# Optimization experiments

Hardware: AMD Instinct MI355X
Metric: run time of the kernel (lower is better)

Reference implementation:

```python
import jax, jax.numpy as jnp
import numpy as np

B, S, H, E, V = 128, 400, 256, 128, 50000
PAD = 250  # extended-vocab padding hard-coded in the torch module


def setup_inputs() -> dict:
    key = jax.random.key(0)
    ks = jax.random.split(key, 20)
    return {
        "input_token": jax.random.randint(ks[0], (B, 1), 0, V),
        "last_decoder_hidden": jax.random.normal(ks[1], (B, H), jnp.float32),
        "encoder_states": jax.random.normal(ks[2], (B, S, H), jnp.float32),
        "full_input_var": jax.random.randint(ks[3], (B, S), 0, V + PAD),
        "emb_table": jax.random.normal(ks[4], (V, E), jnp.float32) * 0.02,
        "gru_w_ih": jax.random.normal(ks[5], (3 * H, E), jnp.float32) * 0.05,
        "gru_w_hh": jax.random.normal(ks[6], (3 * H, H), jnp.float32) * 0.05,
        "gru_b_ih": jax.random.normal(ks[7], (3 * H,), jnp.float32) * 0.05,
        "gru_b_hh": jax.random.normal(ks[8], (3 * H,), jnp.float32) * 0.05,
        "w_h": jax.random.normal(ks[9], (H,), jnp.float32),
        "w_s": jax.random.normal(ks[10], (H,), jnp.float32),
        "att_bias": jax.random.normal(ks[11], (1,), jnp.float32),
        "attn_v": jax.random.normal(ks[12], (H,), jnp.float32),
        "gen_w": jax.random.normal(ks[13], (1, 2 * H + E), jnp.float32) * 0.05,
        "gen_b": jax.random.normal(ks[14], (1,), jnp.float32) * 0.05,
        "outh_w": jax.random.normal(ks[15], (E, 2 * H), jnp.float32) * 0.05,
        "outh_b": jax.random.normal(ks[16], (E,), jnp.float32) * 0.05,
        "outv_w": jax.random.normal(ks[17], (V, E), jnp.float32) * 0.05,
        "outv_b": jax.random.normal(ks[18], (V,), jnp.float32) * 0.05,
    }


def reference(input_token, last_decoder_hidden, encoder_states, full_input_var,
              emb_table, gru_w_ih, gru_w_hh, gru_b_ih, gru_b_hh,
              w_h, w_s, att_bias, attn_v, gen_w, gen_b,
              outh_w, outh_b, outv_w, outv_b):
    b, s, h = encoder_states.shape
    v = outv_w.shape[0]
    # Embedding lookup (dropout is identity in eval mode): [B, E]
    x = emb_table[input_token[:, 0]]
    # Single-step GRU cell (PyTorch gate order: r, z, n)
    gi = x @ gru_w_ih.T + gru_b_ih
    gh = last_decoder_hidden @ gru_w_hh.T + gru_b_hh
    i_r, i_z, i_n = jnp.split(gi, 3, axis=-1)
    h_r, h_z, h_n = jnp.split(gh, 3, axis=-1)
    r = jax.nn.sigmoid(i_r + h_r)
    z = jax.nn.sigmoid(i_z + h_z)
    n = jnp.tanh(i_n + r * h_n)
    h_new = (1.0 - z) * n + z * last_decoder_hidden  # [B, H]
    # Bahdanau-style elementwise attention
    att = jnp.tanh(w_h * encoder_states + w_s * h_new[:, None, :] + att_bias)  # [B,S,H]
    scores = jnp.einsum('bsh,h->bs', att, attn_v)
    att_dist = jax.nn.softmax(scores, axis=-1)  # [B, S]
    context = jnp.einsum('bs,bsh->bh', att_dist, encoder_states)  # [B, H]
    dec_ctx = jnp.concatenate([h_new, context], axis=-1)  # [B, 2H]
    p_vocab = jax.nn.softmax((dec_ctx @ outh_w.T + outh_b) @ outv_w.T + outv_b, axis=-1)  # [B, V]
    p_gen = jax.nn.sigmoid(jnp.concatenate([dec_ctx, x], axis=1) @ gen_w.T + gen_b)  # [B, 1]
    # Pointer scatter-add into extended vocab [B, V+PAD]
    rows = jnp.arange(b)[:, None]
    token_input_dist = jnp.zeros((b, v + PAD), p_vocab.dtype).at[rows, full_input_var].add(att_dist)
    p_final = jnp.concatenate([p_vocab * p_gen, jnp.zeros((b, PAD), p_vocab.dtype)], axis=1) \
              + (1.0 - p_gen) * token_input_dist
    return (h_new, p_final, p_gen, p_vocab, att_dist)
```

## Files before the change

### kernel.cpp

```cpp
#include <hip/hip_runtime.h>
#include <hip/hip_bf16.h>


#define B_ 128
#define S_ 400
#define H_ 256
#define E_ 128
#define V_ 50000
#define PAD_ 250
#define VP_ (V_ + PAD_)
#define NC_ 8
#define CS_ (S_ / NC_)
#define NSUM_ 16

typedef unsigned short ushort_t;
typedef __attribute__((ext_vector_type(8))) short bf16x8;
typedef __attribute__((ext_vector_type(4))) float f32x4;

__device__ __forceinline__ unsigned short f2bfu(float f) {
    __hip_bfloat16 h = __float2bfloat16(f);
    union { __hip_bfloat16 h; unsigned short u; } c;
    c.h = h;
    return c.u;
}

__device__ __forceinline__ float sigmoid_fast(float x) {
    return 1.0f / (1.0f + __expf(-x));
}

__device__ __forceinline__ float tanh_fast(float x) {
    return 1.0f - 2.0f / (__expf(2.0f * x) + 1.0f);
}

__device__ __forceinline__ float waveReduceSumAll(float v) {
#pragma unroll
    for (int off = 1; off < 64; off <<= 1) v += __shfl_xor(v, off, 64);
    return v;
}

__global__ __launch_bounds__(256) void k_gates(
    const int* __restrict__ token, const float* __restrict__ emb,
    const float* __restrict__ hprev,
    const float* __restrict__ w_ih, const float* __restrict__ w_hh,
    float* __restrict__ gi_ws, float* __restrict__ gh_ws,
    float* __restrict__ row_sum16) {
    __shared__ ushort_t xh[B_ * 264];
    __shared__ int toks[B_];
    int t = threadIdx.x;
    bool isIH = blockIdx.x < 12;
    if (blockIdx.x == 0) {
        for (int i = t; i < NSUM_ * B_; i += 256) row_sum16[i] = 0.0f;
    }
    if (isIH) {
        if (t < B_) toks[t] = token[t];
        __syncthreads();
#pragma unroll
        for (int i = 0; i < 16; i++) {
            int fidx = i * 256 + t;
            int b = fidx >> 5, k4 = fidx & 31;
            float4 q = *(const float4*)(emb + (size_t)toks[b] * E_ + k4 * 4);
            ushort4 u;
            u.x = f2bfu(q.x); u.y = f2bfu(q.y); u.z = f2bfu(q.z); u.w = f2bfu(q.w);
            *(ushort4*)&xh[b * 136 + k4 * 4] = u;
        }
    } else {
#pragma unroll
        for (int i = 0; i < 32; i++) {
            int fidx = i * 256 + t;
            int b = fidx >> 6, k4 = fidx & 63;
            float4 q = *(const float4*)(hprev + (size_t)b * H_ + k4 * 4);
            ushort4 u;
            u.x = f2bfu(q.x); u.y = f2bfu(q.y); u.z = f2bfu(q.z); u.w = f2bfu(q.w);
            *(ushort4*)&xh[b * 264 + k4 * 4] = u;
        }
    }
    __syncthreads();

    int wave = t >> 6, lane = t & 63, lm = lane & 15, quad = lane >> 4;
    int tile = (isIH ? blockIdx.x : blockIdx.x - 12) * 4 + wave;
    int v = tile * 16 + lm;
    int K = isIH ? E_ : H_;
    int pitch = isIH ? 136 : 264;
    const float* wrow = (isIH ? w_ih : w_hh) + (size_t)v * K;
    float* gout = isIH ? gi_ws : gh_ws;

    f32x4 acc[8];
#pragma unroll
    for (int bt = 0; bt < 8; bt++) acc[bt] = (f32x4){0.f, 0.f, 0.f, 0.f};

    for (int kc = 0; kc < (K >> 5); kc++) {
        int k0 = kc * 32 + quad * 8;
        float4 w0 = *(const float4*)(wrow + k0);
        float4 w1 = *(const float4*)(wrow + k0 + 4);
        bf16x8 bf;
        bf[0] = (short)f2bfu(w0.x); bf[1] = (short)f2bfu(w0.y);
        bf[2] = (short)f2bfu(w0.z); bf[3] = (short)f2bfu(w0.w);
        bf[4] = (short)f2bfu(w1.x); bf[5] = (short)f2bfu(w1.y);
        bf[6] = (short)f2bfu(w1.z); bf[7] = (short)f2bfu(w1.w);
#pragma unroll
        for (int bt = 0; bt < 8; bt++) {
            bf16x8 af = *(const bf16x8*)&xh[(bt * 16 + lm) * pitch + k0];
            acc[bt] = __builtin_amdgcn_mfma_f32_16x16x32_bf16(af, bf, acc[bt], 0, 0, 0);
        }
    }
#pragma unroll
    for (int bt = 0; bt < 8; bt++)
#pragma unroll
        for (int r = 0; r < 4; r++) {
            int b = bt * 16 + quad * 4 + r;
            gout[(size_t)b * 768 + v] = acc[bt][r];
        }
}

__global__ __launch_bounds__(256) void k_attn(
    const float* __restrict__ gi_ws, const float* __restrict__ gh_ws,
    const float* __restrict__ b_ih, const float* __restrict__ b_hh,
    const float* __restrict__ hprev,
    const float* __restrict__ enc,
    const float* __restrict__ w_h, const float* __restrict__ w_s,
    const float* __restrict__ att_bias, const float* __restrict__ attn_v,
    float* __restrict__ out_hnew,
    float* __restrict__ sc_ws, float* __restrict__ ml_ws, float* __restrict__ ctxp_ws) {
    int c = blockIdx.x, b = blockIdx.y;
    int t = threadIdx.x;
    int wave = t >> 6, lane = t & 63;
    __shared__ float whs[H_], vs[H_], cs[H_], cmerge[H_];
    __shared__ float mred[4], lred[4];

    {
        float ir = gi_ws[(size_t)b * 768 + t] + b_ih[t];
        float iz = gi_ws[(size_t)b * 768 + 256 + t] + b_ih[256 + t];
        float in_ = gi_ws[(size_t)b * 768 + 512 + t] + b_ih[512 + t];
        float hr = gh_ws[(size_t)b * 768 + t] + b_hh[t];
        float hz = gh_ws[(size_t)b * 768 + 256 + t] + b_hh[256 + t];
        float hn = gh_ws[(size_t)b * 768 + 512 + t] + b_hh[512 + t];
        float hp = hprev[(size_t)b * H_ + t];
        float r = sigmoid_fast(ir + hr);
        float z = sigmoid_fast(iz + hz);
        float n = tanh_fast(in_ + r * hn);
        float h = (1.0f - z) * n + z * hp;
        if (c == 0) out_hnew[(size_t)b * H_ + t] = h;
        whs[t] = w_h[t];
        vs[t] = attn_v[t];
        cs[t] = w_s[t] * h + att_bias[0];
        cmerge[t] = 0.0f;
    }
    __syncthreads();

    int h0 = lane * 4;
    float wh0 = whs[h0], wh1 = whs[h0 + 1], wh2 = whs[h0 + 2], wh3 = whs[h0 + 3];
    float vv0 = vs[h0], vv1 = vs[h0 + 1], vv2 = vs[h0 + 2], vv3 = vs[h0 + 3];
    float cc0 = cs[h0], cc1 = cs[h0 + 1], cc2 = cs[h0 + 2], cc3 = cs[h0 + 3];

    float m_w = -1e30f, l_w = 0.0f;
    float cx0 = 0.f, cx1 = 0.f, cx2 = 0.f, cx3 = 0.f;
    for (int si = wave; si < CS_; si += 4) {
        int s = c * CS_ + si;
        float4 u = *(const float4*)(enc + ((size_t)(b * S_ + s)) * H_ + h0);
        float p = vv0 * tanh_fast(wh0 * u.x + cc0)
                + vv1 * tanh_fast(wh1 * u.y + cc1)
                + vv2 * tanh_fast(wh2 * u.z + cc2)
                + vv3 * tanh_fast(wh3 * u.w + cc3);
        p = waveReduceSumAll(p);
        if (lane == 0) sc_ws[b * S_ + s] = p;
        float mn = fmaxf(m_w, p);
        float scale = __expf(m_w - mn);
        float w = __expf(p - mn);
        cx0 = cx0 * scale + w * u.x;
        cx1 = cx1 * scale + w * u.y;
        cx2 = cx2 * scale + w * u.z;
        cx3 = cx3 * scale + w * u.w;
        l_w = l_w * scale + w;
        m_w = mn;
    }
    if (lane == 0) mred[wave] = m_w;
    __syncthreads();
    float m_c = fmaxf(fmaxf(mred[0], mred[1]), fmaxf(mred[2], mred[3]));
    float wf = __expf(m_w - m_c);
    if (lane == 0) lred[wave] = l_w * wf;
    atomicAdd(&cmerge[h0 + 0], cx0 * wf);
    atomicAdd(&cmerge[h0 + 1], cx1 * wf);
    atomicAdd(&cmerge[h0 + 2], cx2 * wf);
    atomicAdd(&cmerge[h0 + 3], cx3 * wf);
    __syncthreads();
    if (t == 0) {
        ml_ws[(b * NC_ + c) * 2 + 0] = m_c;
        ml_ws[(b * NC_ + c) * 2 + 1] = lred[0] + lred[1] + lred[2] + lred[3];
    }
    ctxp_ws[(size_t)(b * NC_ + c) * H_ + t] = cmerge[t];
}

__global__ __launch_bounds__(1024) void k_combine(
    const float* __restrict__ sc_ws, const float* __restrict__ ml_ws,
    const float* __restrict__ ctxp_ws,
    const float* __restrict__ out_hnew,
    const int* __restrict__ token, const float* __restrict__ emb,
    const float* __restrict__ outh_w, const float* __restrict__ outh_b,
    const float* __restrict__ gen_w, const float* __restrict__ gen_b,
    float* __restrict__ out_attd, float* __restrict__ out_pgen,
    ushort_t* __restrict__ hidbf_ws) {
    int b = blockIdx.x;
    int t = threadIdx.x;
    int wave = t >> 6, lane = t & 63;
    __shared__ float ml[NC_ * 2];
    __shared__ float dc[2 * H_ + E_];
    __shared__ float r2[16];

    if (t < NC_ * 2) ml[t] = ml_ws[b * NC_ * 2 + t];
    __syncthreads();
    float M = -1e30f;
#pragma unroll
    for (int c = 0; c < NC_; c++) M = fmaxf(M, ml[2 * c]);
    float L = 0.0f;
#pragma unroll
    for (int c = 0; c < NC_; c++) L += ml[2 * c + 1] * __expf(ml[2 * c] - M);
    float invL = 1.0f / L;

    if (t < S_) {
        out_attd[(size_t)b * S_ + t] = __expf(sc_ws[b * S_ + t] - M) * invL;
    }
    if (t < H_) {
        float acc = 0.0f;
#pragma unroll
        for (int c = 0; c < NC_; c++)
            acc += __expf(ml[2 * c] - M) * ctxp_ws[(size_t)(b * NC_ + c) * H_ + t];
        dc[t] = out_hnew[(size_t)b * H_ + t];
        dc[H_ + t] = acc * invL;
    }
    if (t < E_) dc[2 * H_ + t] = emb[(size_t)token[b] * E_ + t];
    __syncthreads();

    {
        int r = t >> 3, sub = t & 7;
        const float* wrow = outh_w + (size_t)r * (2 * H_);
        float acc = 0.0f;
#pragma unroll
        for (int i = 0; i < 16; i++) {
            int k = i * 32 + sub * 4;
            float4 q = *(const float4*)(wrow + k);
            acc += dc[k] * q.x + dc[k + 1] * q.y + dc[k + 2] * q.z + dc[k + 3] * q.w;
        }
        acc += __shfl_down(acc, 4, 64);
        acc += __shfl_down(acc, 2, 64);
        acc += __shfl_down(acc, 1, 64);
        if (sub == 0) hidbf_ws[(size_t)b * E_ + r] = f2bfu(acc + outh_b[r]);
    }
    float pp = (t < 2 * H_ + E_) ? dc[t] * gen_w[t] : 0.0f;
    pp = waveReduceSumAll(pp);
    if (lane == 0) r2[wave] = pp;
    __syncthreads();
    if (t == 0) {
        float g = 0.0f;
#pragma unroll
        for (int wv = 0; wv < 16; wv++) g += r2[wv];
        out_pgen[b] = sigmoid_fast(g + gen_b[0]);
    }
}

#define VT_TOTAL (V_ / 16)
#define HID_PITCH 136

__device__ __forceinline__ void stage_hid(const ushort_t* __restrict__ hidbf_ws,
                                          ushort_t* __restrict__ hid, int t) {
    const uint4* src = (const uint4*)hidbf_ws;
#pragma unroll
    for (int i = 0; i < 16; i++) {
        int i4 = i * 256 + t;
        uint4 q = src[i4];
        int row = i4 >> 4;
        int col4 = (i4 & 15) * 4;
        *(uint4*)&hid[row * HID_PITCH + col4 * 2] = q;
    }
}

__device__ __forceinline__ void vocab_gemm(const ushort_t* __restrict__ hid,
                                           const float* __restrict__ wrow,
                                           int lm, int quad, f32x4 acc[8]) {
#pragma unroll
    for (int kc = 0; kc < 4; kc++) {
        int k0 = kc * 32 + quad * 8;
        float4 w0 = *(const float4*)(wrow + k0);
        float4 w1 = *(const float4*)(wrow + k0 + 4);
        bf16x8 bf;
        bf[0] = (short)f2bfu(w0.x); bf[1] = (short)f2bfu(w0.y);
        bf[2] = (short)f2bfu(w0.z); bf[3] = (short)f2bfu(w0.w);
        bf[4] = (short)f2bfu(w1.x); bf[5] = (short)f2bfu(w1.y);
        bf[6] = (short)f2bfu(w1.z); bf[7] = (short)f2bfu(w1.w);
#pragma unroll
        for (int bt = 0; bt < 8; bt++) {
            bf16x8 af = *(const bf16x8*)&hid[(bt * 16 + lm) * HID_PITCH + k0];
            acc[bt] = __builtin_amdgcn_mfma_f32_16x16x32_bf16(af, bf, acc[bt], 0, 0, 0);
        }
    }
}

__global__ __launch_bounds__(256) void k_vocab_sum(
    const float* __restrict__ outv_w, const float* __restrict__ outv_b,
    const ushort_t* __restrict__ hidbf_ws,
    float* __restrict__ row_sum16) {
    __shared__ ushort_t hid[B_ * HID_PITCH];
    __shared__ float rsum[B_];
    int t = threadIdx.x;
    stage_hid(hidbf_ws, hid, t);
    if (t < B_) rsum[t] = 0.0f;
    __syncthreads();

    int wave = t >> 6, lane = t & 63, lm = lane & 15, quad = lane >> 4;
    int vt = blockIdx.x * 4 + wave;

    if (vt < VT_TOTAL) {
        int v = vt * 16 + lm;
        const float* wrow = outv_w + (size_t)v * E_;
        f32x4 acc[8];
#pragma unroll
        for (int bt = 0; bt < 8; bt++) acc[bt] = (f32x4){0.f, 0.f, 0.f, 0.f};
        vocab_gemm(hid, wrow, lm, quad, acc);

        float bias = outv_b[v];
#pragma unroll
        for (int bt = 0; bt < 8; bt++) {
#pragma unroll
            for (int r = 0; r < 4; r++) {
                int b = bt * 16 + quad * 4 + r;
                float e = __expf(fminf(acc[bt][r] + bias, 60.0f));
                float s = e;
                s += __shfl_xor(s, 1);
                s += __shfl_xor(s, 2);
                s += __shfl_xor(s, 4);
                s += __shfl_xor(s, 8);
                if (lm == 0) atomicAdd(&rsum[b], s);
            }
        }
    }
    __syncthreads();
    if (t < B_) atomicAdd(&row_sum16[(blockIdx.x & (NSUM_ - 1)) * B_ + t], rsum[t]);
}

__global__ __launch_bounds__(256) void k_vocab_write(
    const float* __restrict__ outv_w, const float* __restrict__ outv_b,
    const ushort_t* __restrict__ hidbf_ws,
    const float* __restrict__ row_sum16, const float* __restrict__ pgen,
    float* __restrict__ out_pvocab, float* __restrict__ out_pfinal) {
    __shared__ ushort_t hid[B_ * HID_PITCH];
    __shared__ float rsinv[B_], pgs[B_];
    int t = threadIdx.x;
    stage_hid(hidbf_ws, hid, t);
    if (t < B_) {
        float rs = 0.0f;
#pragma unroll
        for (int i = 0; i < NSUM_; i++) rs += row_sum16[i * B_ + t];
        rsinv[t] = 1.0f / rs;
        pgs[t] = pgen[t];
    }
    __syncthreads();

    int wave = t >> 6, lane = t & 63, lm = lane & 15, quad = lane >> 4;
    int vt = blockIdx.x * 4 + wave;

    if (vt < VT_TOTAL) {
        int v = vt * 16 + lm;
        const float* wrow = outv_w + (size_t)v * E_;
        f32x4 acc[8];
#pragma unroll
        for (int bt = 0; bt < 8; bt++) acc[bt] = (f32x4){0.f, 0.f, 0.f, 0.f};
        vocab_gemm(hid, wrow, lm, quad, acc);

        float bias = outv_b[v];
#pragma unroll
        for (int bt = 0; bt < 8; bt++) {
#pragma unroll
            for (int r = 0; r < 4; r++) {
                int b = bt * 16 + quad * 4 + r;
                float e = __expf(fminf(acc[bt][r] + bias, 60.0f));
                float p = e * rsinv[b];
                out_pvocab[(size_t)b * V_ + v] = p;
                out_pfinal[(size_t)b * VP_ + v] = p * pgs[b];
            }
        }
    }
}

__global__ __launch_bounds__(256) void k_scatter(
    const int* __restrict__ fiv, const float* __restrict__ attd,
    const float* __restrict__ pgen, float* __restrict__ out_pfinal) {
    int b = blockIdx.x;
    int t = threadIdx.x;
    float* pfrow = out_pfinal + (size_t)b * VP_;
    if (t < PAD_) pfrow[V_ + t] = 0.0f;
    __syncthreads();
    float omg = 1.0f - pgen[b];
    for (int s = t; s < S_; s += 256) {
        int idx = fiv[b * S_ + s];
        atomicAdd(&pfrow[idx], omg * attd[(size_t)b * S_ + s]);
    }
}

extern "C" void kernel_launch(void* const* d_in, const int* in_sizes, int n_in,
                              void* d_out, int out_size, void* d_ws, size_t ws_size,
                              hipStream_t stream) {
    const int* token = (const int*)d_in[0];
    const float* hprev = (const float*)d_in[1];
    const float* enc = (const float*)d_in[2];
    const int* fiv = (const int*)d_in[3];
    const float* emb = (const float*)d_in[4];
    const float* w_ih = (const float*)d_in[5];
    const float* w_hh = (const float*)d_in[6];
    const float* b_ih = (const float*)d_in[7];
    const float* b_hh = (const float*)d_in[8];
    const float* w_h = (const float*)d_in[9];
    const float* w_s = (const float*)d_in[10];
    const float* att_bias = (const float*)d_in[11];
    const float* attn_v = (const float*)d_in[12];
    const float* gen_w = (const float*)d_in[13];
    const float* gen_b = (const float*)d_in[14];
    const float* outh_w = (const float*)d_in[15];
    const float* outh_b = (const float*)d_in[16];
    const float* outv_w = (const float*)d_in[17];
    const float* outv_b = (const float*)d_in[18];

    float* out = (float*)d_out;
    float* out_hnew = out;
    float* out_pfinal = out + (size_t)B_ * H_;
    float* out_pgen = out_pfinal + (size_t)B_ * VP_;
    float* out_pvocab = out_pgen + B_;
    float* out_attd = out_pvocab + (size_t)B_ * V_;

    float* wsf = (float*)d_ws;
    float* gi_ws = wsf;
    float* gh_ws = wsf + 98304;
    float* row_sum16 = wsf + 196608;
    float* sc_ws = wsf + 198656;
    float* ml_ws = wsf + 249856;
    float* ctxp_ws = wsf + 251904;
    ushort_t* hidbf_ws = (ushort_t*)(wsf + 514048);

    k_gates<<<24, 256, 0, stream>>>(token, emb, hprev, w_ih, w_hh,
                                    gi_ws, gh_ws, row_sum16);
    k_attn<<<dim3(NC_, B_), 256, 0, stream>>>(gi_ws, gh_ws, b_ih, b_hh, hprev,
                                              enc, w_h, w_s, att_bias, attn_v,
                                              out_hnew, sc_ws, ml_ws, ctxp_ws);
    k_combine<<<B_, 1024, 0, stream>>>(sc_ws, ml_ws, ctxp_ws, out_hnew, token, emb,
                                       outh_w, outh_b, gen_w, gen_b,
                                       out_attd, out_pgen, hidbf_ws);
    k_vocab_sum<<<782, 256, 0, stream>>>(outv_w, outv_b, hidbf_ws, row_sum16);
    k_vocab_write<<<782, 256, 0, stream>>>(outv_w, outv_b, hidbf_ws,
                                           row_sum16, out_pgen,
                                           out_pvocab, out_pfinal);
    k_scatter<<<B_, 256, 0, stream>>>(fiv, out_attd, out_pgen, out_pfinal);
}
```

Measured before the change: 227.0 us.

## Fuse attention and combine kernels into one block per batch row

Merges the split attention kernel (8 chunks per row) and the combine kernel into a single 1024-thread block per batch row. The softmax merge and context now stay in shared memory instead of going through workspace buffers, which removes one launch and the global round-trip. The sequence loop is also batched in groups of 7 rows, so loads are issued before the reductions and more memory traffic is in flight. The trade is a smaller grid (128 blocks instead of 1024) for streaming the 52MB encoder tensor, which may leave much of the device idle.

New measurement: 241.1 us. 1.06x slower.

```diff
diff --git a/kernel.cpp b/kernel.cpp
--- a/kernel.cpp
+++ b/kernel.cpp
@@ -9,9 +9,9 @@
 #define V_ 50000
 #define PAD_ 250
 #define VP_ (V_ + PAD_)
-#define NC_ 8
-#define CS_ (S_ / NC_)
 #define NSUM_ 16
+#define SPW_ 25
+#define SB_ 7
 
 typedef unsigned short ushort_t;
 typedef __attribute__((ext_vector_type(8))) short bf16x8;
@@ -112,22 +112,28 @@
         }
 }
 
-__global__ __launch_bounds__(256) void k_attn(
+__global__ __launch_bounds__(1024) void k_attn_combine(
     const float* __restrict__ gi_ws, const float* __restrict__ gh_ws,
     const float* __restrict__ b_ih, const float* __restrict__ b_hh,
     const float* __restrict__ hprev,
     const float* __restrict__ enc,
     const float* __restrict__ w_h, const float* __restrict__ w_s,
     const float* __restrict__ att_bias, const float* __restrict__ attn_v,
-    float* __restrict__ out_hnew,
-    float* __restrict__ sc_ws, float* __restrict__ ml_ws, float* __restrict__ ctxp_ws) {
-    int c = blockIdx.x, b = blockIdx.y;
+    const int* __restrict__ token, const float* __restrict__ emb,
+    const float* __restrict__ outh_w, const float* __restrict__ outh_b,
+    const float* __restrict__ gen_w, const float* __restrict__ gen_b,
+    float* __restrict__ out_hnew, float* __restrict__ out_attd,
+    float* __restrict__ out_pgen,
+    ushort_t* __restrict__ hidbf_ws) {
+    int b = blockIdx.x;
     int t = threadIdx.x;
     int wave = t >> 6, lane = t & 63;
     __shared__ float whs[H_], vs[H_], cs[H_], cmerge[H_];
-    __shared__ float mred[4], lred[4];
-
-    {
+    __shared__ float scl[S_];
+    __shared__ float mred[16], lred[16], r2[16];
+    __shared__ float dc[2 * H_ + E_];
+
+    if (t < H_) {
         float ir = gi_ws[(size_t)b * 768 + t] + b_ih[t];
         float iz = gi_ws[(size_t)b * 768 + 256 + t] + b_ih[256 + t];
         float in_ = gi_ws[(size_t)b * 768 + 512 + t] + b_ih[512 + t];
@@ -139,12 +145,14 @@
         float z = sigmoid_fast(iz + hz);
         float n = tanh_fast(in_ + r * hn);
         float h = (1.0f - z) * n + z * hp;
-        if (c == 0) out_hnew[(size_t)b * H_ + t] = h;
+        out_hnew[(size_t)b * H_ + t] = h;
+        dc[t] = h;
         whs[t] = w_h[t];
         vs[t] = attn_v[t];
         cs[t] = w_s[t] * h + att_bias[0];
         cmerge[t] = 0.0f;
     }
+    if (t < E_) dc[2 * H_ + t] = emb[(size_t)token[b] * E_ + t];
     __syncthreads();
 
     int h0 = lane * 4;
@@ -152,82 +160,80 @@
     float vv0 = vs[h0], vv1 = vs[h0 + 1], vv2 = vs[h0 + 2], vv3 = vs[h0 + 3];
     float cc0 = cs[h0], cc1 = cs[h0 + 1], cc2 = cs[h0 + 2], cc3 = cs[h0 + 3];
 
+    int s0 = wave * SPW_;
     float m_w = -1e30f, l_w = 0.0f;
     float cx0 = 0.f, cx1 = 0.f, cx2 = 0.f, cx3 = 0.f;
-    for (int si = wave; si < CS_; si += 4) {
-        int s = c * CS_ + si;
-        float4 u = *(const float4*)(enc + ((size_t)(b * S_ + s)) * H_ + h0);
-        float p = vv0 * tanh_fast(wh0 * u.x + cc0)
-                + vv1 * tanh_fast(wh1 * u.y + cc1)
-                + vv2 * tanh_fast(wh2 * u.z + cc2)
-                + vv3 * tanh_fast(wh3 * u.w + cc3);
-        p = waveReduceSumAll(p);
-        if (lane == 0) sc_ws[b * S_ + s] = p;
-        float mn = fmaxf(m_w, p);
+#pragma unroll
+    for (int jb = 0; jb < 4; jb++) {
+        int nb = (jb < 3) ? SB_ : (SPW_ - 3 * SB_);
+        float4 u[SB_];
+        float p[SB_];
+#pragma unroll
+        for (int i = 0; i < SB_; i++) {
+            if (i < nb) {
+                int s = s0 + jb * SB_ + i;
+                u[i] = *(const float4*)(enc + ((size_t)(b * S_ + s)) * H_ + h0);
+            }
+        }
+#pragma unroll
+        for (int i = 0; i < SB_; i++) {
+            if (i < nb) {
+                p[i] = vv0 * tanh_fast(wh0 * u[i].x + cc0)
+                     + vv1 * tanh_fast(wh1 * u[i].y + cc1)
+                     + vv2 * tanh_fast(wh2 * u[i].z + cc2)
+                     + vv3 * tanh_fast(wh3 * u[i].w + cc3);
+            }
+        }
+#pragma unroll
+        for (int i = 0; i < SB_; i++) {
+            if (i < nb) p[i] = waveReduceSumAll(p[i]);
+        }
+        if (lane == 0) {
+#pragma unroll
+            for (int i = 0; i < SB_; i++)
+                if (i < nb) scl[s0 + jb * SB_ + i] = p[i];
+        }
+        float mb = -1e30f;
+#pragma unroll
+        for (int i = 0; i < SB_; i++)
+            if (i < nb) mb = fmaxf(mb, p[i]);
+        float mn = fmaxf(m_w, mb);
         float scale = __expf(m_w - mn);
-        float w = __expf(p - mn);
-        cx0 = cx0 * scale + w * u.x;
-        cx1 = cx1 * scale + w * u.y;
-        cx2 = cx2 * scale + w * u.z;
-        cx3 = cx3 * scale + w * u.w;
-        l_w = l_w * scale + w;
+        float wsum = 0.f, a0 = 0.f, a1 = 0.f, a2 = 0.f, a3 = 0.f;
+#pragma unroll
+        for (int i = 0; i < SB_; i++) {
+            if (i < nb) {
+                float wi = __expf(p[i] - mn);
+                wsum += wi;
+                a0 += wi * u[i].x; a1 += wi * u[i].y;
+                a2 += wi * u[i].z; a3 += wi * u[i].w;
+            }
+        }
+        cx0 = cx0 * scale + a0; cx1 = cx1 * scale + a1;
+        cx2 = cx2 * scale + a2; cx3 = cx3 * scale + a3;
+        l_w = l_w * scale + wsum;
         m_w = mn;
     }
+
     if (lane == 0) mred[wave] = m_w;
     __syncthreads();
-    float m_c = fmaxf(fmaxf(mred[0], mred[1]), fmaxf(mred[2], mred[3]));
-    float wf = __expf(m_w - m_c);
+    float M = -1e30f;
+#pragma unroll
+    for (int i = 0; i < 16; i++) M = fmaxf(M, mred[i]);
+    float wf = __expf(m_w - M);
     if (lane == 0) lred[wave] = l_w * wf;
     atomicAdd(&cmerge[h0 + 0], cx0 * wf);
     atomicAdd(&cmerge[h0 + 1], cx1 * wf);
     atomicAdd(&cmerge[h0 + 2], cx2 * wf);
     atomicAdd(&cmerge[h0 + 3], cx3 * wf);
     __syncthreads();
-    if (t == 0) {
-        ml_ws[(b * NC_ + c) * 2 + 0] = m_c;
-        ml_ws[(b * NC_ + c) * 2 + 1] = lred[0] + lred[1] + lred[2] + lred[3];
-    }
-    ctxp_ws[(size_t)(b * NC_ + c) * H_ + t] = cmerge[t];
-}
-
-__global__ __launch_bounds__(1024) void k_combine(
-    const float* __restrict__ sc_ws, const float* __restrict__ ml_ws,
-    const float* __restrict__ ctxp_ws,
-    const float* __restrict__ out_hnew,
-    const int* __restrict__ token, const float* __restrict__ emb,
-    const float* __restrict__ outh_w, const float* __restrict__ outh_b,
-    const float* __restrict__ gen_w, const float* __restrict__ gen_b,
-    float* __restrict__ out_attd, float* __restrict__ out_pgen,
-    ushort_t* __restrict__ hidbf_ws) {
-    int b = blockIdx.x;
-    int t = threadIdx.x;
-    int wave = t >> 6, lane = t & 63;
-    __shared__ float ml[NC_ * 2];
-    __shared__ float dc[2 * H_ + E_];
-    __shared__ float r2[16];
-
-    if (t < NC_ * 2) ml[t] = ml_ws[b * NC_ * 2 + t];
-    __syncthreads();
-    float M = -1e30f;
-#pragma unroll
-    for (int c = 0; c < NC_; c++) M = fmaxf(M, ml[2 * c]);
     float L = 0.0f;
 #pragma unroll
-    for (int c = 0; c < NC_; c++) L += ml[2 * c + 1] * __expf(ml[2 * c] - M);
+    for (int i = 0; i < 16; i++) L += lred[i];
     float invL = 1.0f / L;
 
-    if (t < S_) {
-        out_attd[(size_t)b * S_ + t] = __expf(sc_ws[b * S_ + t] - M) * invL;
-    }
-    if (t < H_) {
-        float acc = 0.0f;
-#pragma unroll
-        for (int c = 0; c < NC_; c++)
-            acc += __expf(ml[2 * c] - M) * ctxp_ws[(size_t)(b * NC_ + c) * H_ + t];
-        dc[t] = out_hnew[(size_t)b * H_ + t];
-        dc[H_ + t] = acc * invL;
-    }
-    if (t < E_) dc[2 * H_ + t] = emb[(size_t)token[b] * E_ + t];
+    if (t < S_) out_attd[(size_t)b * S_ + t] = __expf(scl[t] - M) * invL;
+    if (t < H_) dc[H_ + t] = cmerge[t] * invL;
     __syncthreads();
 
     {
@@ -429,19 +435,14 @@
     float* gi_ws = wsf;
     float* gh_ws = wsf + 98304;
     float* row_sum16 = wsf + 196608;
-    float* sc_ws = wsf + 198656;
-    float* ml_ws = wsf + 249856;
-    float* ctxp_ws = wsf + 251904;
-    ushort_t* hidbf_ws = (ushort_t*)(wsf + 514048);
+    ushort_t* hidbf_ws = (ushort_t*)(wsf + 198656);
 
     k_gates<<<24, 256, 0, stream>>>(token, emb, hprev, w_ih, w_hh,
                                     gi_ws, gh_ws, row_sum16);
-    k_attn<<<dim3(NC_, B_), 256, 0, stream>>>(gi_ws, gh_ws, b_ih, b_hh, hprev,
-                                              enc, w_h, w_s, att_bias, attn_v,
-                                              out_hnew, sc_ws, ml_ws, ctxp_ws);
-    k_combine<<<B_, 1024, 0, stream>>>(sc_ws, ml_ws, ctxp_ws, out_hnew, token, emb,
-                                       outh_w, outh_b, gen_w, gen_b,
-                                       out_attd, out_pgen, hidbf_ws);
+    k_attn_combine<<<B_, 1024, 0, stream>>>(gi_ws, gh_ws, b_ih, b_hh, hprev,
+                                            enc, w_h, w_s, att_bias, attn_v,
+                                            token, emb, outh_w, outh_b, gen_w, gen_b,
+                                            out_hnew, out_attd, out_pgen, hidbf_ws);
     k_vocab_sum<<<782, 256, 0, stream>>>(outv_w, outv_b, hidbf_ws, row_sum16);
     k_vocab_write<<<782, 256, 0, stream>>>(outv_w, outv_b, hidbf_ws,
                                            row_sum16, out_pgen,
```

## Fold pointer scatter into combine kernel and accumulate into pre-zeroed p_final

Applied to the files above, without the earlier changes.

Removes the separate scatter kernel. The attention kernel now zero-fills the whole p_final buffer, the combine kernel scatter-adds (1-p_gen)*att_dist into it, and the vocab write kernel accumulates its p_vocab*p_gen term onto the existing value. This saves a launch and a dependency stage, but adds a full zero-fill pass and a read-modify-write of the large p_final buffer.

Measured after the change: 231.1 us. About the same (+1.8%).

```diff
diff --git a/kernel.cpp b/kernel.cpp
--- a/kernel.cpp
+++ b/kernel.cpp
@@ -120,12 +120,20 @@
     const float* __restrict__ w_h, const float* __restrict__ w_s,
     const float* __restrict__ att_bias, const float* __restrict__ attn_v,
     float* __restrict__ out_hnew,
-    float* __restrict__ sc_ws, float* __restrict__ ml_ws, float* __restrict__ ctxp_ws) {
+    float* __restrict__ sc_ws, float* __restrict__ ml_ws, float* __restrict__ ctxp_ws,
+    float* __restrict__ out_pfinal) {
     int c = blockIdx.x, b = blockIdx.y;
     int t = threadIdx.x;
     int wave = t >> 6, lane = t & 63;
     __shared__ float whs[H_], vs[H_], cs[H_], cmerge[H_];
     __shared__ float mred[4], lred[4];
+
+    {
+        int gid = (c * gridDim.y + b) * 256 + t;
+        float4* pf4 = (float4*)out_pfinal;
+        const float4 z = {0.f, 0.f, 0.f, 0.f};
+        for (int i = gid; i < (B_ * VP_ / 4); i += NC_ * B_ * 256) pf4[i] = z;
+    }
 
     {
         float ir = gi_ws[(size_t)b * 768 + t] + b_ih[t];
@@ -197,14 +205,16 @@
     const int* __restrict__ token, const float* __restrict__ emb,
     const float* __restrict__ outh_w, const float* __restrict__ outh_b,
     const float* __restrict__ gen_w, const float* __restrict__ gen_b,
+    const int* __restrict__ fiv,
     float* __restrict__ out_attd, float* __restrict__ out_pgen,
-    ushort_t* __restrict__ hidbf_ws) {
+    ushort_t* __restrict__ hidbf_ws, float* __restrict__ out_pfinal) {
     int b = blockIdx.x;
     int t = threadIdx.x;
     int wave = t >> 6, lane = t & 63;
     __shared__ float ml[NC_ * 2];
     __shared__ float dc[2 * H_ + E_];
     __shared__ float r2[16];
+    __shared__ float pg_sh;
 
     if (t < NC_ * 2) ml[t] = ml_ws[b * NC_ * 2 + t];
     __syncthreads();
@@ -216,8 +226,10 @@
     for (int c = 0; c < NC_; c++) L += ml[2 * c + 1] * __expf(ml[2 * c] - M);
     float invL = 1.0f / L;
 
+    float a = 0.0f;
     if (t < S_) {
-        out_attd[(size_t)b * S_ + t] = __expf(sc_ws[b * S_ + t] - M) * invL;
+        a = __expf(sc_ws[b * S_ + t] - M) * invL;
+        out_attd[(size_t)b * S_ + t] = a;
     }
     if (t < H_) {
         float acc = 0.0f;
@@ -253,7 +265,14 @@
         float g = 0.0f;
 #pragma unroll
         for (int wv = 0; wv < 16; wv++) g += r2[wv];
-        out_pgen[b] = sigmoid_fast(g + gen_b[0]);
+        g = sigmoid_fast(g + gen_b[0]);
+        out_pgen[b] = g;
+        pg_sh = g;
+    }
+    __syncthreads();
+    if (t < S_) {
+        int idx = fiv[b * S_ + t];
+        atomicAdd(&out_pfinal[(size_t)b * VP_ + idx], (1.0f - pg_sh) * a);
     }
 }
 
@@ -374,24 +393,10 @@
                 float e = __expf(fminf(acc[bt][r] + bias, 60.0f));
                 float p = e * rsinv[b];
                 out_pvocab[(size_t)b * V_ + v] = p;
-                out_pfinal[(size_t)b * VP_ + v] = p * pgs[b];
+                size_t fi = (size_t)b * VP_ + v;
+                out_pfinal[fi] = p * pgs[b] + out_pfinal[fi];
             }
         }
-    }
-}
-
-__global__ __launch_bounds__(256) void k_scatter(
-    const int* __restrict__ fiv, const float* __restrict__ attd,
-    const float* __restrict__ pgen, float* __restrict__ out_pfinal) {
-    int b = blockIdx.x;
-    int t = threadIdx.x;
-    float* pfrow = out_pfinal + (size_t)b * VP_;
-    if (t < PAD_) pfrow[V_ + t] = 0.0f;
-    __syncthreads();
-    float omg = 1.0f - pgen[b];
-    for (int s = t; s < S_; s += 256) {
-        int idx = fiv[b * S_ + s];
-        atomicAdd(&pfrow[idx], omg * attd[(size_t)b * S_ + s]);
     }
 }
 
@@ -438,13 +443,13 @@
                                     gi_ws, gh_ws, row_sum16);
     k_attn<<<dim3(NC_, B_), 256, 0, stream>>>(gi_ws, gh_ws, b_ih, b_hh, hprev,
                                               enc, w_h, w_s, att_bias, attn_v,
-                                              out_hnew, sc_ws, ml_ws, ctxp_ws);
+                                              out_hnew, sc_ws, ml_ws, ctxp_ws,
+                                              out_pfinal);
     k_combine<<<B_, 1024, 0, stream>>>(sc_ws, ml_ws, ctxp_ws, out_hnew, token, emb,
-                                       outh_w, outh_b, gen_w, gen_b,
-                                       out_attd, out_pgen, hidbf_ws);
+                                       outh_w, outh_b, gen_w, gen_b, fiv,
+                                       out_attd, out_pgen, hidbf_ws, out_pfinal);
     k_vocab_sum<<<782, 256, 0, stream>>>(outv_w, outv_b, hidbf_ws, row_sum16);
     k_vocab_write<<<782, 256, 0, stream>>>(outv_w, outv_b, hidbf_ws,
                                            row_sum16, out_pgen,
                                            out_pvocab, out_pfinal);
-    k_scatter<<<B_, 256, 0, stream>>>(fiv, out_attd, out_pgen, out_pfinal);
-}
+}
```
